# Optimization experiments

Hardware: AMD Instinct MI355X
Metric: run time of the kernel (lower is better)

## Reference

```python
import jax, jax.numpy as jnp
import numpy as np

N_RAYS = 131072
N_SAMPLES = 64
N_IMP = 64
NEAR, FAR = 2.0, 6.0
EPS_W = 1e-5
EPS_T = 1e-10
FAR_DIST = 1e10


def setup_inputs() -> dict:
    key = jax.random.key(0)
    k = jax.random.split(key, 6)
    ro = jax.random.normal(k[0], (N_RAYS, 3), dtype=jnp.float32)
    rd = jax.random.normal(k[1], (N_RAYS, 3), dtype=jnp.float32)
    ev = jax.random.uniform(k[2], (N_RAYS, 1), dtype=jnp.float32)
    Wd = jax.random.normal(k[3], (3, 1), dtype=jnp.float32) * 0.5
    Wc = jax.random.normal(k[4], (3, 3), dtype=jnp.float32) * 0.5
    aid = jax.random.randint(k[5], (N_RAYS,), 0, 1000)
    return {"ray_origins": ro, "ray_directions": rd, "exposure_values": ev,
            "Wd": Wd, "Wc": Wc, "appearance_ids": aid}


def _query_model(pos, Wd, Wc):
    # stand-in BlockNeRF field: density [N,S], color [N,S,3]
    density = jax.nn.softplus(pos @ Wd)[..., 0]
    color = jax.nn.sigmoid(pos @ Wc)
    return density, color


def _compute_weights(density, t_vals):
    dists = t_vals[..., 1:] - t_vals[..., :-1]
    dists = jnp.concatenate([dists, jnp.full_like(dists[..., :1], FAR_DIST)], axis=-1)
    alpha = 1.0 - jnp.exp(-density * dists)
    trans = jnp.cumprod(
        jnp.concatenate([jnp.ones_like(alpha[..., :1]), 1.0 - alpha[..., :-1] + EPS_T], axis=-1),
        axis=-1)
    return alpha * trans


def _composite(weights, colors, t_vals):
    rgb = jnp.sum(weights[..., None] * colors, axis=-2)
    depth = jnp.sum(weights * t_vals, axis=-1)
    acc = jnp.sum(weights, axis=-1)
    rgb = rgb + (1.0 - acc[..., None])  # white background
    return rgb, depth, acc


def _hierarchical_tvals(t_vals, weights):
    # inverse-CDF importance sampling (deterministic u since eval mode)
    w = weights + EPS_W
    pdf = w / jnp.sum(w, axis=-1, keepdims=True)
    cdf = jnp.cumsum(pdf, axis=-1)
    cdf = jnp.concatenate([jnp.zeros_like(cdf[..., :1]), cdf], axis=-1)  # [N, S+1]
    u = jnp.linspace(0.0, 1.0, N_IMP, dtype=cdf.dtype)                   # [Simp]
    idx = jax.vmap(lambda c: jnp.searchsorted(c, u, side='right'))(cdf)  # [N, Simp]
    S1 = cdf.shape[-1]
    below = jnp.clip(idx - 1, 0, S1 - 1)
    above = jnp.clip(idx, 0, S1 - 1)
    cdf0 = jnp.take_along_axis(cdf, below, axis=-1)
    cdf1 = jnp.take_along_axis(cdf, above, axis=-1)
    Sb = t_vals.shape[-1]
    bin0 = jnp.take_along_axis(t_vals, jnp.clip(below, 0, Sb - 1), axis=-1)
    bin1 = jnp.take_along_axis(t_vals, jnp.clip(above, 0, Sb - 1), axis=-1)
    denom = cdf1 - cdf0
    denom = jnp.where(denom < EPS_W, jnp.ones_like(denom), denom)
    t = (u - cdf0) / denom
    t_samples = bin0 + t * (bin1 - bin0)
    return jnp.sort(jnp.concatenate([t_vals, t_samples], axis=-1), axis=-1)  # [N, S+Simp]


def reference(ray_origins, ray_directions, exposure_values, Wd, Wc, appearance_ids):
    N = ray_origins.shape[0]
    t_lin = jnp.linspace(0.0, 1.0, N_SAMPLES, dtype=ray_origins.dtype)
    t_vals = jnp.broadcast_to(NEAR + (FAR - NEAR) * t_lin, (N, N_SAMPLES))
    pos = ray_origins[:, None, :] + ray_directions[:, None, :] * t_vals[..., None]
    density, color = _query_model(pos, Wd, Wc)
    weights = _compute_weights(density, t_vals)
    rgb, depth, acc = _composite(weights, color, t_vals)
    # fine pass
    ft = _hierarchical_tvals(t_vals, weights)
    fpos = ray_origins[:, None, :] + ray_directions[:, None, :] * ft[..., None]
    fdens, fcol = _query_model(fpos, Wd, Wc)
    fw = _compute_weights(fdens, ft)
    frgb, fdepth, facc = _composite(fw, fcol, ft)
    return rgb, depth, acc, frgb, fdepth, facc
```

## Files before the change

kernel.cpp:

```cpp
#include <hip/hip_runtime.h>
#include <math.h>

#define NEAR_T   2.0f
#define FAR_T    6.0f
#define EPS_W_C  1e-5f
#define EPS_T_C  1e-10f
#define FAR_DIST 1e10f
#define L2E      1.4426950408889634f
#define INV63    (1.0f / 63.0f)

typedef float v2f __attribute__((ext_vector_type(2)));

__device__ __forceinline__ float tval(int i) {
    return NEAR_T + (FAR_T - NEAR_T) * ((float)i * INV63);
}
__device__ __forceinline__ float rcp_fast(float x) { return __builtin_amdgcn_rcpf(x); }
__device__ __forceinline__ float exp2_f(float x)  { return __builtin_amdgcn_exp2f(x); }
__device__ __forceinline__ float log2_f(float x)  { return __builtin_amdgcn_logf(x); }
__device__ __forceinline__ v2f fma2(v2f a, v2f b, v2f c) {
    return __builtin_elementwise_fma(a, b, c);
}

__device__ __forceinline__ float softplus2_safe(float xp) {
    const float e = exp2_f(-fabsf(xp));
    const float big   = log2_f(1.0f + e);
    const float small = e * (1.4426950f - e * (0.72134751f - e * 0.48089835f));
    return fmaxf(xp, 0.0f) + ((e > 0.0078125f) ? big : small);
}

struct FieldV { float sig; float c2; v2f c01; };

__device__ __forceinline__ FieldV eval_fast(float t, v2f A0, v2f A1, v2f B0, v2f B1) {
    const v2f tt = {t, t};
    const v2f a = fma2(tt, A1, A0);
    const v2f b = fma2(tt, B1, B0);
    const float ea  = exp2_f(-fabsf(a.x));
    const float ec  = exp2_f(-a.y);
    const float eb0 = exp2_f(-b.x);
    const float eb1 = exp2_f(-b.y);
    const v2f pa = (v2f){ea, ec} + (v2f){1.0f, 1.0f};
    const v2f pb = (v2f){eb0, eb1} + (v2f){1.0f, 1.0f};
    FieldV r;
    r.sig = fmaxf(a.x, 0.0f) + log2_f(pa.x);
    r.c2  = rcp_fast(pa.y);
    r.c01 = (v2f){rcp_fast(pb.x), rcp_fast(pb.y)};
    return r;
}

__global__ __launch_bounds__(256)
void volrender_tpr(const float* __restrict__ ro_g,
                   const float* __restrict__ rd_g,
                   const float* __restrict__ Wd_g,
                   const float* __restrict__ Wc_g,
                   float* __restrict__ out, int N) {
    __shared__ float s_cdf[64][256];

    const int tid = threadIdx.x;
    const int ray = blockIdx.x * 256 + tid;
    if (ray >= N) return;

    const float ox = ro_g[ray * 3 + 0], oy = ro_g[ray * 3 + 1], oz = ro_g[ray * 3 + 2];
    const float dx = rd_g[ray * 3 + 0], dy = rd_g[ray * 3 + 1], dz = rd_g[ray * 3 + 2];
    const float wd0 = Wd_g[0], wd1 = Wd_g[1], wd2 = Wd_g[2];
    float wcm[9];
#pragma unroll
    for (int k = 0; k < 9; ++k) wcm[k] = Wc_g[k];

    const v2f A0 = { (ox * wd0 + oy * wd1 + oz * wd2) * L2E,
                     (ox * wcm[2] + oy * wcm[5] + oz * wcm[8]) * L2E };
    const v2f A1 = { (dx * wd0 + dy * wd1 + dz * wd2) * L2E,
                     (dx * wcm[2] + dy * wcm[5] + dz * wcm[8]) * L2E };
    const v2f B0 = { (ox * wcm[0] + oy * wcm[3] + oz * wcm[6]) * L2E,
                     (ox * wcm[1] + oy * wcm[4] + oz * wcm[7]) * L2E };
    const v2f B1 = { (dx * wcm[0] + dy * wcm[3] + dz * wcm[6]) * L2E,
                     (dx * wcm[1] + dy * wcm[4] + dz * wcm[7]) * L2E };

    const float W = (FAR_T - NEAR_T) * INV63;
    const float TMAX = tval(63);

    const long Nl = N;
    float* out_rgb  = out;
    float* out_dep  = out + 3 * Nl;
    float* out_acc  = out + 4 * Nl;
    float* out_frgb = out + 5 * Nl;
    float* out_fdep = out + 8 * Nl;
    float* out_facc = out + 9 * Nl;

    float q  = exp2_f(fmaf(NEAR_T, A1.x, A0.x));
    float z2 = exp2_f(-fmaf(NEAR_T, A1.y, A0.y));
    float z0 = exp2_f(-fmaf(NEAR_T, B1.x, B0.x));
    float z1 = exp2_f(-fmaf(NEAR_T, B1.y, B0.y));
    const float Kq  = exp2_f(A1.x * W);
    const float Kz2 = exp2_f(-A1.y * W);
    const float Kz0 = exp2_f(-B1.x * W);
    const float Kz1 = exp2_f(-B1.y * W);

    float S1 = 0.0f, Tp1 = 1.0f;
    float acc = 0.0f, dep = 0.0f, r2 = 0.0f, total = 0.0f;
    v2f r01 = {0.0f, 0.0f};
    float t = NEAR_T;
#pragma unroll 4
    for (int i = 0; i < 63; ++i) {
        const float sig = log2_f(1.0f + q);
        const float c0 = rcp_fast(1.0f + z0);
        const float c1 = rcp_fast(1.0f + z1);
        const float c2 = rcp_fast(1.0f + z2);
        S1 = fmaf(sig, W, S1);
        const float T = exp2_f(-S1);
        const float w = Tp1 - T;
        Tp1 = T;
        acc += w; dep = fmaf(w, t, dep);
        r01 = fma2((v2f){w, w}, (v2f){c0, c1}, r01);
        r2 = fmaf(w, c2, r2);
        total += w + EPS_W_C;
        s_cdf[i][tid] = total;
        t += W;
        q *= Kq; z0 *= Kz0; z1 *= Kz1; z2 *= Kz2;
    }
    {
        const float sig = softplus2_safe(fmaf(t, A1.x, A0.x));
        const float c0 = rcp_fast(1.0f + z0);
        const float c1 = rcp_fast(1.0f + z1);
        const float c2 = rcp_fast(1.0f + z2);
        S1 = fmaf(sig, FAR_DIST, S1);
        const float T = exp2_f(-S1);
        const float w = Tp1 - T;
        acc += w; dep = fmaf(w, t, dep);
        r01 = fma2((v2f){w, w}, (v2f){c0, c1}, r01);
        r2 = fmaf(w, c2, r2);
        total += w + EPS_W_C;
        s_cdf[63][tid] = total;
    }
    {
        const float bg = 1.0f - acc;
        out_rgb[ray * 3 + 0] = r01.x + bg;
        out_rgb[ray * 3 + 1] = r01.y + bg;
        out_rgb[ray * 3 + 2] = r2 + bg;
        out_dep[ray] = dep;
        out_acc[ray] = acc;
    }
    const float inv_total = rcp_fast(total);

    float Sf = 0.0f, Tpf = 1.0f;
    float facc = 0.0f, fdep = 0.0f, fr2 = 0.0f;
    v2f fr01 = {0.0f, 0.0f};
    float lo, hi, bin0, bin1, binw;
    int i, j = 0;
    float u = 0.0f;
    float pt, ps, pc2;
    v2f pc01;
    float Snext;

    {
        const FieldV F = eval_fast(NEAR_T, A0, A1, B0, B1);
        ps = F.sig; pc01 = F.c01; pc2 = F.c2; pt = NEAR_T;
        lo = 0.0f;
        hi = s_cdf[0][tid] * inv_total;
        bin0 = NEAR_T; bin1 = NEAR_T + W; binw = bin1 - bin0;
        i = 1;
        Snext = s_cdf[1][tid];
    }

#pragma unroll 4
    for (int e = 1; e < 128; ++e) {
        float dnm = hi - lo;
        dnm = (dnm < EPS_W_C) ? 1.0f : dnm;
        const float ts = fmaf((u - lo) * rcp_fast(dnm), binw, bin0);
        const bool samp = (j < 64) && ((i >= 64) || (u < hi));
        const float tm = samp ? ts : bin1;

        const FieldV F = eval_fast(tm, A0, A1, B0, B1);

        Sf = fmaf(ps, tm - pt, Sf);
        const float T = exp2_f(-Sf);
        const float wf = Tpf - T;
        Tpf = T;
        facc += wf; fdep = fmaf(wf, pt, fdep);
        fr01 = fma2((v2f){wf, wf}, pc01, fr01);
        fr2 = fmaf(wf, pc2, fr2);

        if (samp) {
            ++j; u += INV63;
        } else {
            lo = hi;
            hi = Snext * inv_total;
            bin0 = bin1;
            bin1 = fminf(bin1 + W, TMAX);
            binw = bin1 - bin0;
            ++i;
            Snext = s_cdf[min(i, 63)][tid];
        }
        pt = tm; ps = F.sig; pc01 = F.c01; pc2 = F.c2;
    }

    {
        const float sig = softplus2_safe(fmaf(pt, A1.x, A0.x));
        Sf = fmaf(sig, FAR_DIST, Sf);
        const float T = exp2_f(-Sf);
        const float wf = Tpf - T;
        facc += wf; fdep = fmaf(wf, pt, fdep);
        fr01 = fma2((v2f){wf, wf}, pc01, fr01);
        fr2 = fmaf(wf, pc2, fr2);

        const float bg = 1.0f - facc;
        out_frgb[ray * 3 + 0] = fr01.x + bg;
        out_frgb[ray * 3 + 1] = fr01.y + bg;
        out_frgb[ray * 3 + 2] = fr2 + bg;
        out_fdep[ray] = fdep;
        out_facc[ray] = facc;
    }
}

extern "C" void kernel_launch(void* const* d_in, const int* in_sizes, int n_in,
                              void* d_out, int out_size, void* d_ws, size_t ws_size,
                              hipStream_t stream) {
    const float* ro = (const float*)d_in[0];
    const float* rd = (const float*)d_in[1];
    const float* Wd = (const float*)d_in[3];
    const float* Wc = (const float*)d_in[4];
    float* out = (float*)d_out;

    const int N = in_sizes[0] / 3;
    const int grid = (N + 255) / 256;
    volrender_tpr<<<grid, 256, 0, stream>>>(ro, rd, Wd, Wc, out, N);
}
```

Before: 42.93 us.

## Split each ray across two threads with transmittance-scaled merge of halves

Each ray is now processed by a pair of adjacent lanes. Each lane handles half of the coarse samples and half of the fine merged-sample loop. The second lane finds its starting point in the merge with a binary search over the CDF and shifts its partial CDF by the first lane's transmittance. Partial composites are combined with shuffles weighted by the first half's transmittance. This doubles the thread count to improve latency hiding and halves each thread's serial chain, at the cost of extra shuffles, a block barrier, the binary-search setup and duplicated per-ray setup.

Result: no change. 43.22 us (+0.7%).

```diff
diff --git a/kernel.cpp b/kernel.cpp
--- a/kernel.cpp
+++ b/kernel.cpp
@@ -20,6 +20,7 @@
 __device__ __forceinline__ v2f fma2(v2f a, v2f b, v2f c) {
     return __builtin_elementwise_fma(a, b, c);
 }
+__device__ __forceinline__ float shfx1(float v) { return __shfl_xor(v, 1); }
 
 __device__ __forceinline__ float softplus2_safe(float xp) {
     const float e = exp2_f(-fabsf(xp));
@@ -47,17 +48,19 @@
     return r;
 }
 
-__global__ __launch_bounds__(256)
-void volrender_tpr(const float* __restrict__ ro_g,
-                   const float* __restrict__ rd_g,
-                   const float* __restrict__ Wd_g,
-                   const float* __restrict__ Wc_g,
-                   float* __restrict__ out, int N) {
-    __shared__ float s_cdf[64][256];
+__global__ __launch_bounds__(256, 4)
+void volrender_tpr2(const float* __restrict__ ro_g,
+                    const float* __restrict__ rd_g,
+                    const float* __restrict__ Wd_g,
+                    const float* __restrict__ Wc_g,
+                    float* __restrict__ out, int N) {
+    __shared__ float s_cdf[64][128];
 
     const int tid = threadIdx.x;
-    const int ray = blockIdx.x * 256 + tid;
-    if (ray >= N) return;
+    const int col = tid >> 1;
+    const int isB = tid & 1;
+    int ray = blockIdx.x * 128 + col;
+    if (ray >= N) ray = N - 1;
 
     const float ox = ro_g[ray * 3 + 0], oy = ro_g[ray * 3 + 1], oz = ro_g[ray * 3 + 2];
     const float dx = rd_g[ray * 3 + 0], dy = rd_g[ray * 3 + 1], dz = rd_g[ray * 3 + 2];
@@ -86,128 +89,199 @@
     float* out_fdep = out + 8 * Nl;
     float* out_facc = out + 9 * Nl;
 
-    float q  = exp2_f(fmaf(NEAR_T, A1.x, A0.x));
-    float z2 = exp2_f(-fmaf(NEAR_T, A1.y, A0.y));
-    float z0 = exp2_f(-fmaf(NEAR_T, B1.x, B0.x));
-    float z1 = exp2_f(-fmaf(NEAR_T, B1.y, B0.y));
+    const float tstart = fmaf(isB ? 32.0f : 0.0f, W, NEAR_T);
+    float q  = exp2_f(fmaf(tstart, A1.x, A0.x));
+    float z2 = exp2_f(-fmaf(tstart, A1.y, A0.y));
+    float z0 = exp2_f(-fmaf(tstart, B1.x, B0.x));
+    float z1 = exp2_f(-fmaf(tstart, B1.y, B0.y));
     const float Kq  = exp2_f(A1.x * W);
     const float Kz2 = exp2_f(-A1.y * W);
     const float Kz0 = exp2_f(-B1.x * W);
     const float Kz1 = exp2_f(-B1.y * W);
 
     float S1 = 0.0f, Tp1 = 1.0f;
-    float acc = 0.0f, dep = 0.0f, r2 = 0.0f, total = 0.0f;
+    float acc = 0.0f, dep = 0.0f, r2 = 0.0f, total = 0.0f, sumw = 0.0f;
     v2f r01 = {0.0f, 0.0f};
-    float t = NEAR_T;
+    float t = tstart;
+    const int rowbase = isB ? 32 : 0;
 #pragma unroll 4
-    for (int i = 0; i < 63; ++i) {
+    for (int k = 0; k < 31; ++k) {
         const float sig = log2_f(1.0f + q);
         const float c0 = rcp_fast(1.0f + z0);
         const float c1 = rcp_fast(1.0f + z1);
         const float c2 = rcp_fast(1.0f + z2);
         S1 = fmaf(sig, W, S1);
         const float T = exp2_f(-S1);
-        const float w = Tp1 - T;
-        Tp1 = T;
+        const float w = Tp1 - T; Tp1 = T;
         acc += w; dep = fmaf(w, t, dep);
         r01 = fma2((v2f){w, w}, (v2f){c0, c1}, r01);
         r2 = fmaf(w, c2, r2);
         total += w + EPS_W_C;
-        s_cdf[i][tid] = total;
+        sumw  += w;
+        s_cdf[rowbase + k][col] = isB ? sumw : total;
         t += W;
         q *= Kq; z0 *= Kz0; z1 *= Kz1; z2 *= Kz2;
     }
     {
-        const float sig = softplus2_safe(fmaf(t, A1.x, A0.x));
+        const float sig = isB ? softplus2_safe(fmaf(t, A1.x, A0.x)) : log2_f(1.0f + q);
         const float c0 = rcp_fast(1.0f + z0);
         const float c1 = rcp_fast(1.0f + z1);
         const float c2 = rcp_fast(1.0f + z2);
-        S1 = fmaf(sig, FAR_DIST, S1);
+        const float dist = isB ? FAR_DIST : W;
+        S1 = fmaf(sig, dist, S1);
         const float T = exp2_f(-S1);
-        const float w = Tp1 - T;
+        const float w = Tp1 - T; Tp1 = T;
         acc += w; dep = fmaf(w, t, dep);
         r01 = fma2((v2f){w, w}, (v2f){c0, c1}, r01);
         r2 = fmaf(w, c2, r2);
         total += w + EPS_W_C;
-        s_cdf[63][tid] = total;
-    }
-    {
-        const float bg = 1.0f - acc;
-        out_rgb[ray * 3 + 0] = r01.x + bg;
-        out_rgb[ray * 3 + 1] = r01.y + bg;
-        out_rgb[ray * 3 + 2] = r2 + bg;
-        out_dep[ray] = dep;
-        out_acc[ray] = acc;
-    }
-    const float inv_total = rcp_fast(total);
+        sumw += w;
+        s_cdf[rowbase + 31][col] = isB ? sumw : total;
+    }
+
+    const float TA   = shfx1(Tp1);
+    const float cdfA = shfx1(total);
+    float total_g;
+    {
+        const float tgB = fmaf(TA, sumw, cdfA) + 32.0f * EPS_W_C;
+        const float tgA = shfx1(tgB);
+        total_g = isB ? tgB : tgA;
+    }
+    {
+        const float bacc = shfx1(acc), bdep = shfx1(dep), br2 = shfx1(r2);
+        const float br0 = shfx1(r01.x), br1 = shfx1(r01.y);
+        if (!isB) {
+            const float ga = fmaf(Tp1, bacc, acc);
+            const float gd = fmaf(Tp1, bdep, dep);
+            const float g0 = fmaf(Tp1, br0, r01.x);
+            const float g1 = fmaf(Tp1, br1, r01.y);
+            const float g2 = fmaf(Tp1, br2, r2);
+            const float bg = 1.0f - ga;
+            out_rgb[ray * 3 + 0] = g0 + bg;
+            out_rgb[ray * 3 + 1] = g1 + bg;
+            out_rgb[ray * 3 + 2] = g2 + bg;
+            out_dep[ray] = gd;
+            out_acc[ray] = ga;
+        }
+    }
+    if (isB) {
+        float ebase = cdfA + EPS_W_C;
+#pragma unroll 4
+        for (int k = 0; k < 32; ++k) {
+            const float raw = s_cdf[32 + k][col];
+            s_cdf[32 + k][col] = fmaf(TA, raw, ebase);
+            ebase += EPS_W_C;
+        }
+    }
+    __syncthreads();
+    const float inv_total = rcp_fast(total_g);
 
     float Sf = 0.0f, Tpf = 1.0f;
     float facc = 0.0f, fdep = 0.0f, fr2 = 0.0f;
     v2f fr01 = {0.0f, 0.0f};
-    float lo, hi, bin0, bin1, binw;
-    int i, j = 0;
-    float u = 0.0f;
-    float pt, ps, pc2;
-    v2f pc01;
-    float Snext;
-
-    {
+    float lo, hi, bin0, bin1, binw, jf, Snext;
+    int i;
+    float pt, ps, pc2; v2f pc01;
+
+    if (!isB) {
         const FieldV F = eval_fast(NEAR_T, A0, A1, B0, B1);
-        ps = F.sig; pc01 = F.c01; pc2 = F.c2; pt = NEAR_T;
-        lo = 0.0f;
-        hi = s_cdf[0][tid] * inv_total;
+        pt = NEAR_T; ps = F.sig; pc01 = F.c01; pc2 = F.c2;
+        i = 1; jf = 0.0f;
+        lo = 0.0f; hi = s_cdf[0][col] * inv_total;
         bin0 = NEAR_T; bin1 = NEAR_T + W; binw = bin1 - bin0;
-        i = 1;
-        Snext = s_cdf[1][tid];
+        Snext = s_cdf[1][col];
+    } else {
+        int loI = 1, hiI = 64;
+        while (loI < hiI) {
+            const int mid = (loI + hiI) >> 1;
+            const float c = s_cdf[mid - 1][col] * inv_total;
+            int k = (int)(c * 63.0f);
+            k = min(max(k, 0), 64);
+#pragma unroll
+            for (int f = 0; f < 3; ++f) if (k > 0 && (float)(k - 1) * INV63 >= c) --k;
+#pragma unroll
+            for (int f = 0; f < 3; ++f) if (k < 64 && (float)k * INV63 < c) ++k;
+            if (mid + k >= 64) hiI = mid; else loI = mid + 1;
+        }
+        const int i0 = loI;
+        jf = (float)(64 - i0);
+        lo = (i0 >= 2) ? s_cdf[i0 - 2][col] * inv_total : 0.0f;
+        hi = s_cdf[i0 - 1][col] * inv_total;
+        bin1 = fminf(fmaf((float)i0, W, NEAR_T), TMAX);
+        bin0 = fminf(fmaf((float)(i0 - 1), W, NEAR_T), TMAX);
+        binw = bin1 - bin0;
+        i = i0;
+        Snext = s_cdf[min(i0, 63)][col];
+        float dnm = hi - lo; dnm = (dnm < EPS_W_C) ? 1.0f : dnm;
+        const float u = jf * INV63;
+        const float ts = fmaf((u - lo) * rcp_fast(dnm), binw, bin0);
+        const bool samp = (jf < 63.5f) && ((i >= 64) || (u < hi));
+        const float tm = samp ? ts : bin1;
+        const FieldV F = eval_fast(tm, A0, A1, B0, B1);
+        if (samp) { jf += 1.0f; }
+        else {
+            lo = hi; hi = Snext * inv_total;
+            bin0 = bin1; bin1 = fminf(bin1 + W, TMAX); binw = bin1 - bin0;
+            ++i; Snext = s_cdf[min(i, 63)][col];
+        }
+        pt = tm; ps = F.sig; pc01 = F.c01; pc2 = F.c2;
     }
 
 #pragma unroll 4
-    for (int e = 1; e < 128; ++e) {
-        float dnm = hi - lo;
-        dnm = (dnm < EPS_W_C) ? 1.0f : dnm;
+    for (int e = 0; e < 63; ++e) {
+        float dnm = hi - lo; dnm = (dnm < EPS_W_C) ? 1.0f : dnm;
+        const float u = jf * INV63;
         const float ts = fmaf((u - lo) * rcp_fast(dnm), binw, bin0);
-        const bool samp = (j < 64) && ((i >= 64) || (u < hi));
+        const bool samp = (jf < 63.5f) && ((i >= 64) || (u < hi));
         const float tm = samp ? ts : bin1;
-
         const FieldV F = eval_fast(tm, A0, A1, B0, B1);
-
         Sf = fmaf(ps, tm - pt, Sf);
         const float T = exp2_f(-Sf);
-        const float wf = Tpf - T;
-        Tpf = T;
+        const float wf = Tpf - T; Tpf = T;
         facc += wf; fdep = fmaf(wf, pt, fdep);
         fr01 = fma2((v2f){wf, wf}, pc01, fr01);
         fr2 = fmaf(wf, pc2, fr2);
-
-        if (samp) {
-            ++j; u += INV63;
-        } else {
-            lo = hi;
-            hi = Snext * inv_total;
-            bin0 = bin1;
-            bin1 = fminf(bin1 + W, TMAX);
-            binw = bin1 - bin0;
-            ++i;
-            Snext = s_cdf[min(i, 63)][tid];
+        if (samp) { jf += 1.0f; }
+        else {
+            lo = hi; hi = Snext * inv_total;
+            bin0 = bin1; bin1 = fminf(bin1 + W, TMAX); binw = bin1 - bin0;
+            ++i; Snext = s_cdf[min(i, 63)][col];
         }
         pt = tm; ps = F.sig; pc01 = F.c01; pc2 = F.c2;
     }
-
-    {
-        const float sig = softplus2_safe(fmaf(pt, A1.x, A0.x));
-        Sf = fmaf(sig, FAR_DIST, Sf);
+    {
+        float dnm = hi - lo; dnm = (dnm < EPS_W_C) ? 1.0f : dnm;
+        const float u = jf * INV63;
+        const float ts = fmaf((u - lo) * rcp_fast(dnm), binw, bin0);
+        const bool samp = (jf < 63.5f) && ((i >= 64) || (u < hi));
+        const float tm = samp ? ts : bin1;
+        const float sig_safe = softplus2_safe(fmaf(pt, A1.x, A0.x));
+        const float ps_e = isB ? sig_safe : ps;
+        const float dist = isB ? FAR_DIST : (tm - pt);
+        Sf = fmaf(ps_e, dist, Sf);
         const float T = exp2_f(-Sf);
         const float wf = Tpf - T;
         facc += wf; fdep = fmaf(wf, pt, fdep);
         fr01 = fma2((v2f){wf, wf}, pc01, fr01);
         fr2 = fmaf(wf, pc2, fr2);
-
-        const float bg = 1.0f - facc;
-        out_frgb[ray * 3 + 0] = fr01.x + bg;
-        out_frgb[ray * 3 + 1] = fr01.y + bg;
-        out_frgb[ray * 3 + 2] = fr2 + bg;
-        out_fdep[ray] = fdep;
-        out_facc[ray] = facc;
+    }
+    {
+        const float TFA = exp2_f(-Sf);
+        const float bfacc = shfx1(facc), bfdep = shfx1(fdep), bfr2 = shfx1(fr2);
+        const float bf0 = shfx1(fr01.x), bf1 = shfx1(fr01.y);
+        if (!isB) {
+            const float ga = fmaf(TFA, bfacc, facc);
+            const float gd = fmaf(TFA, bfdep, fdep);
+            const float g0 = fmaf(TFA, bf0, fr01.x);
+            const float g1 = fmaf(TFA, bf1, fr01.y);
+            const float g2 = fmaf(TFA, bfr2, fr2);
+            const float bg = 1.0f - ga;
+            out_frgb[ray * 3 + 0] = g0 + bg;
+            out_frgb[ray * 3 + 1] = g1 + bg;
+            out_frgb[ray * 3 + 2] = g2 + bg;
+            out_fdep[ray] = gd;
+            out_facc[ray] = ga;
+        }
     }
 }
 
@@ -221,6 +295,6 @@
     float* out = (float*)d_out;
 
     const int N = in_sizes[0] / 3;
-    const int grid = (N + 255) / 256;
-    volrender_tpr<<<grid, 256, 0, stream>>>(ro, rd, Wd, Wc, out, N);
-}
+    const int grid = (2 * N + 255) / 256;
+    volrender_tpr2<<<grid, 256, 0, stream>>>(ro, rd, Wd, Wc, out, N);
+}
```
